# Performance work log

Measured on AMD Instinct MI355X. Metric: run time of the kernel, lower is better.

## Reference

```python
import jax, jax.numpy as jnp
import numpy as np

MODES = 16
WIDTH = 64
SCHMIDT = 8
N_LAYERS = 4


def _spectral_conv(x, wr, wi, modes):
    """Quantum spectral conv: truncated 2D FFT -> complex Schmidt-rank einsum -> inverse FFT.
    x: (B,H,W,C) real. wr, wi: (modes,modes,C,C,S)."""
    b, H, W, C = x.shape
    S = wr.shape[-1]
    # quantum_fourier_modes: keep low (modes x modes) Fourier modes
    x_ft = jnp.fft.fftn(x, axes=(1, 2))[:, :modes, :modes, :]          # (B,m,n,C) complex
    w = wr + 1j * wi                                                     # (m,n,C,C,S)
    # tensor_product_einsum('b...nc,mncos->b...mos')
    out_ft = jnp.einsum('bxnc,mncos->bxmos', x_ft, w)                   # (B,m,m,C,S)
    # recombine Schmidt components (normalized sum over rank)
    out_ft = out_ft.sum(axis=-1) * (1.0 / float(np.sqrt(S)))            # (B,m,m,C)
    full = jnp.zeros((b, H, W, C), dtype=x_ft.dtype).at[:, :modes, :modes, :].set(out_ft)
    # inverse quantum_fourier_modes + .real
    return jnp.fft.ifftn(full, axes=(1, 2)).real


def setup_inputs() -> dict:
    key = jax.random.key(0)
    ks = jax.random.split(key, 12)
    B, H, W, Cin = 16, 128, 128, 3
    sc = 0.02
    inp = {
        'x': jax.random.normal(ks[0], (B, H, W, Cin), jnp.float32),
        'fc_in_w': jax.random.normal(ks[1], (Cin, WIDTH), jnp.float32) * sc,
        'fc_in_b': jnp.zeros((WIDTH,), jnp.float32),
        'wr': jax.random.normal(ks[2], (N_LAYERS, MODES, MODES, WIDTH, WIDTH, SCHMIDT), jnp.float32) * sc,
        'wi': jax.random.normal(ks[3], (N_LAYERS, MODES, MODES, WIDTH, WIDTH, SCHMIDT), jnp.float32) * sc,
        'ww': jax.random.normal(ks[4], (N_LAYERS, WIDTH, WIDTH), jnp.float32) * sc,
        'wb': jnp.zeros((N_LAYERS, WIDTH), jnp.float32),
        'fc1_w': jax.random.normal(ks[5], (WIDTH, 128), jnp.float32) * sc,
        'fc1_b': jnp.zeros((128,), jnp.float32),
        'fc2_w': jax.random.normal(ks[6], (128, 1), jnp.float32) * sc,
        'fc2_b': jnp.zeros((1,), jnp.float32),
    }
    return inp


def reference(x, fc_in_w, fc_in_b, wr, wi, ww, wb, fc1_w, fc1_b, fc2_w, fc2_b) -> jnp.ndarray:
    h = x @ fc_in_w + fc_in_b                                   # (B,H,W,width)
    for i in range(N_LAYERS):
        x1 = _spectral_conv(h, wr[i], wi[i], MODES)             # quantum spectral path
        x2 = h @ ww[i] + wb[i]                                  # pointwise Dense path
        h = jax.nn.gelu(x1 + x2)
    h = jax.nn.gelu(h @ fc1_w + fc1_b)
    return h @ fc2_w + fc2_b                                    # (B,H,W,1)
```

## Files before the change

### kernel.cpp

```cpp
#include <hip/hip_runtime.h>
#include <math.h>


#define TWO_PI_128 0.049087385212340517f

__device__ __forceinline__ float gelu_f(float v) {
  float ex = 1.5957691216057308f * v * fmaf(0.044715f, v * v, 1.0f);
  float e = __expf(fminf(ex, 30.0f));
  float r = __builtin_amdgcn_rcpf(e + 1.0f);
  return fmaf(-v, r, v);
}

__global__ __launch_bounds__(256) void k_fc_in(const float* __restrict__ x,
    const float* __restrict__ w, const float* __restrict__ b,
    float* __restrict__ h) {
  int t = blockIdx.x * 256 + threadIdx.x;
  int pix = t >> 4, c4 = (t & 15) << 2;
  float x0 = x[pix * 3], x1 = x[pix * 3 + 1], x2 = x[pix * 3 + 2];
  float4 acc = *(const float4*)&b[c4];
  float4 w0 = *(const float4*)&w[c4];
  float4 w1 = *(const float4*)&w[64 + c4];
  float4 w2 = *(const float4*)&w[128 + c4];
  acc.x = fmaf(x2, w2.x, fmaf(x1, w1.x, fmaf(x0, w0.x, acc.x)));
  acc.y = fmaf(x2, w2.y, fmaf(x1, w1.y, fmaf(x0, w0.y, acc.y)));
  acc.z = fmaf(x2, w2.z, fmaf(x1, w1.z, fmaf(x0, w0.z, acc.z)));
  acc.w = fmaf(x2, w2.w, fmaf(x1, w1.w, fmaf(x0, w0.w, acc.w)));
  *(float4*)&h[(size_t)pix * 64 + c4] = acc;
}

__global__ __launch_bounds__(256) void k_prep(const float* __restrict__ wr,
    const float* __restrict__ wi, float* __restrict__ Br, float* __restrict__ Bi) {
  int t = blockIdx.x * 256 + threadIdx.x;
  int o = t & 63, c = (t >> 6) & 63, n = (t >> 12) & 15, m = t >> 16;
  const float4* pr = (const float4*)(wr) + (size_t)t * 2;
  float4 a = pr[0], d = pr[1];
  float sr = ((a.x + a.y) + (a.z + a.w)) + ((d.x + d.y) + (d.z + d.w));
  const float4* pi = (const float4*)(wi) + (size_t)t * 2;
  a = pi[0]; d = pi[1];
  float si = ((a.x + a.y) + (a.z + a.w)) + ((d.x + d.y) + (d.z + d.w));
  const float scale = 0.35355339059327373f / 16384.0f;
  int k = n * 64 + c, j = m * 64 + o;
  Br[k * 1024 + j] = sr * scale;
  Bi[k * 1024 + j] = si * scale;
}

__global__ __launch_bounds__(256) void k_dft_y(const float* __restrict__ h,
                                               float2* __restrict__ A1) {
  __shared__ float sh[128 * 64];
  int bx = blockIdx.x;
  const float* src = h + (size_t)bx * 8192;
  for (int i = threadIdx.x; i < 2048; i += 256)
    *(float4*)&sh[i * 4] = *(const float4*)&src[i * 4];
  __syncthreads();
  int c = threadIdx.x & 63, kg = threadIdx.x >> 6;
  float s4r[4][4], s4i[4][4];
  float w4r[4], w4i[4], c4t[4], s4t[4];
  #pragma unroll
  for (int q = 0; q < 4; ++q) {
    int ky = kg + 4 * q;
    __sincosf(-TWO_PI_128 * 4.0f * (float)ky, &s4t[q], &c4t[q]);
    w4r[q] = 1.f; w4i[q] = 0.f;
    #pragma unroll
    for (int p = 0; p < 4; ++p) { s4r[q][p] = 0.f; s4i[q][p] = 0.f; }
  }
  for (int m = 0; m < 32; ++m) {
    float hv[4];
    #pragma unroll
    for (int p = 0; p < 4; ++p) hv[p] = sh[(4 * m + p) * 64 + c];
    #pragma unroll
    for (int q = 0; q < 4; ++q) {
      #pragma unroll
      for (int p = 0; p < 4; ++p) {
        s4r[q][p] = fmaf(hv[p], w4r[q], s4r[q][p]);
        s4i[q][p] = fmaf(hv[p], w4i[q], s4i[q][p]);
      }
      float nw = w4r[q] * c4t[q] - w4i[q] * s4t[q];
      w4i[q] = fmaf(w4i[q], c4t[q], w4r[q] * s4t[q]);
      w4r[q] = nw;
    }
  }
  #pragma unroll
  for (int q = 0; q < 4; ++q) {
    int ky = kg + 4 * q;
    float s1, c1;
    __sincosf(-TWO_PI_128 * (float)ky, &s1, &c1);
    float sr = s4r[q][0], si = s4i[q][0];
    float wr_ = c1, wi_ = s1;
    #pragma unroll
    for (int p = 1; p < 4; ++p) {
      sr = fmaf(s4r[q][p], wr_, sr); sr = fmaf(-s4i[q][p], wi_, sr);
      si = fmaf(s4r[q][p], wi_, si); si = fmaf(s4i[q][p], wr_, si);
      float nw = wr_ * c1 - wi_ * s1;
      wi_ = fmaf(wi_, c1, wr_ * s1);
      wr_ = nw;
    }
    A1[((size_t)bx * 16 + ky) * 64 + c] = make_float2(sr, si);
  }
}

__global__ __launch_bounds__(256) void k_dft_x(const float2* __restrict__ A1,
    float* __restrict__ Ar, float* __restrict__ Ai) {
  __shared__ float2 sh[128 * 32];
  int b = blockIdx.x, ky = blockIdx.y, ch = blockIdx.z;
  int c0 = ch * 32;
  for (int i = threadIdx.x; i < 2048; i += 256) {
    int xx = i >> 4, u = (i & 15) * 2;
    *(float4*)&sh[xx * 32 + u] =
        *(const float4*)&A1[(((size_t)b * 128 + xx) * 16 + ky) * 64 + c0 + u];
  }
  __syncthreads();
  int cl = threadIdx.x & 31, kxg = threadIdx.x >> 5;
  float cs[2], sn[2], wr_[2], wi_[2], sr[2], si[2];
  #pragma unroll
  for (int q = 0; q < 2; ++q) {
    int kx = kxg + 8 * q;
    __sincosf(-TWO_PI_128 * (float)kx, &sn[q], &cs[q]);
    wr_[q] = 1.f; wi_[q] = 0.f; sr[q] = 0.f; si[q] = 0.f;
  }
  for (int xx = 0; xx < 128; ++xx) {
    float2 v = sh[xx * 32 + cl];
    #pragma unroll
    for (int q = 0; q < 2; ++q) {
      sr[q] = fmaf(v.x, wr_[q], sr[q]); sr[q] = fmaf(-v.y, wi_[q], sr[q]);
      si[q] = fmaf(v.x, wi_[q], si[q]); si[q] = fmaf(v.y, wr_[q], si[q]);
      float nw = wr_[q] * cs[q] - wi_[q] * sn[q];
      wi_[q] = fmaf(wi_[q], cs[q], wr_[q] * sn[q]);
      wr_[q] = nw;
    }
  }
  #pragma unroll
  for (int q = 0; q < 2; ++q) {
    int kx = kxg + 8 * q;
    int row = b * 16 + kx, col = ky * 64 + c0 + cl;
    Ar[row * 1024 + col] = sr[q];
    Ai[row * 1024 + col] = si[q];
  }
}

#define CMAC(cr, ci, ax, ay, bx, by)                 \
  cr = fmaf(ax, bx, cr); cr = fmaf(-(ay), by, cr);   \
  ci = fmaf(ax, by, ci); ci = fmaf(ay, bx, ci);

__global__ __launch_bounds__(256) void k_gemm(const float* __restrict__ Ar,
    const float* __restrict__ Ai, const float* __restrict__ Br,
    const float* __restrict__ Bi, float2* __restrict__ Cp) {
  __shared__ float2 As[2][32][34];
  __shared__ float2 Bs[2][32][34];
  int tx = threadIdx.x & 15, ty = threadIdx.x >> 4;
  int row0 = blockIdx.y * 32, col0 = blockIdx.x * 32, kbase = blockIdx.z * 512;
  int ra = threadIdx.x >> 3, k4 = (threadIdx.x & 7) << 2;
  float4 arv, aiv, brv, biv;
  float cr00 = 0, cr01 = 0, cr10 = 0, cr11 = 0;
  float ci00 = 0, ci01 = 0, ci10 = 0, ci11 = 0;
  {
    int gia = (row0 + ra) * 1024 + kbase + k4;
    arv = *(const float4*)&Ar[gia];
    aiv = *(const float4*)&Ai[gia];
    int gib = (kbase + ra) * 1024 + col0 + k4;
    brv = *(const float4*)&Br[gib];
    biv = *(const float4*)&Bi[gib];
    *(float4*)&As[0][ra][k4]     = make_float4(arv.x, aiv.x, arv.y, aiv.y);
    *(float4*)&As[0][ra][k4 + 2] = make_float4(arv.z, aiv.z, arv.w, aiv.w);
    *(float4*)&Bs[0][ra][k4]     = make_float4(brv.x, biv.x, brv.y, biv.y);
    *(float4*)&Bs[0][ra][k4 + 2] = make_float4(brv.z, biv.z, brv.w, biv.w);
  }
  __syncthreads();
  for (int kt = 0; kt < 16; ++kt) {
    if (kt < 15) {
      int k0 = kbase + (kt + 1) * 32;
      int gia = (row0 + ra) * 1024 + k0 + k4;
      arv = *(const float4*)&Ar[gia];
      aiv = *(const float4*)&Ai[gia];
      int gib = (k0 + ra) * 1024 + col0 + k4;
      brv = *(const float4*)&Br[gib];
      biv = *(const float4*)&Bi[gib];
    }
    int cur = kt & 1;
    #pragma unroll 8
    for (int kk2 = 0; kk2 < 16; ++kk2) {
      float4 a0p = *(const float4*)&As[cur][ty * 2][kk2 * 2];
      float4 a1p = *(const float4*)&As[cur][ty * 2 + 1][kk2 * 2];
      float4 b0p = *(const float4*)&Bs[cur][kk2 * 2][tx * 2];
      float4 b1p = *(const float4*)&Bs[cur][kk2 * 2 + 1][tx * 2];
      CMAC(cr00, ci00, a0p.x, a0p.y, b0p.x, b0p.y)
      CMAC(cr01, ci01, a0p.x, a0p.y, b0p.z, b0p.w)
      CMAC(cr10, ci10, a1p.x, a1p.y, b0p.x, b0p.y)
      CMAC(cr11, ci11, a1p.x, a1p.y, b0p.z, b0p.w)
      CMAC(cr00, ci00, a0p.z, a0p.w, b1p.x, b1p.y)
      CMAC(cr01, ci01, a0p.z, a0p.w, b1p.z, b1p.w)
      CMAC(cr10, ci10, a1p.z, a1p.w, b1p.x, b1p.y)
      CMAC(cr11, ci11, a1p.z, a1p.w, b1p.z, b1p.w)
    }
    __syncthreads();
    if (kt < 15) {
      int nxt = cur ^ 1;
      *(float4*)&As[nxt][ra][k4]     = make_float4(arv.x, aiv.x, arv.y, aiv.y);
      *(float4*)&As[nxt][ra][k4 + 2] = make_float4(arv.z, aiv.z, arv.w, aiv.w);
      *(float4*)&Bs[nxt][ra][k4]     = make_float4(brv.x, biv.x, brv.y, biv.y);
      *(float4*)&Bs[nxt][ra][k4 + 2] = make_float4(brv.z, biv.z, brv.w, biv.w);
    }
    __syncthreads();
  }
  int r = row0 + ty * 2, jj = col0 + tx * 2;
  size_t base = ((size_t)blockIdx.z * 256 + r) * 1024 + jj;
  Cp[base]        = make_float2(cr00, ci00);
  Cp[base + 1]    = make_float2(cr01, ci01);
  Cp[base + 1024] = make_float2(cr10, ci10);
  Cp[base + 1025] = make_float2(cr11, ci11);
}

__global__ __launch_bounds__(256) void k_ifft_y(const float2* __restrict__ Cp,
                                                float2* __restrict__ T) {
  __shared__ float2 Cl[1024];
  int b = blockIdx.x >> 4, kx = blockIdx.x & 15;
  int row = b * 16 + kx;
  for (int i = threadIdx.x; i < 512; i += 256) {
    float4 u = *(const float4*)&Cp[(size_t)row * 1024 + i * 2];
    float4 v = *(const float4*)&Cp[(size_t)(256 + row) * 1024 + i * 2];
    *(float4*)&Cl[i * 2] = make_float4(u.x + v.x, u.y + v.y, u.z + v.z, u.w + v.w);
  }
  __syncthreads();
  int c = threadIdx.x & 63, yg = threadIdx.x >> 6;
  for (int y = yg; y < 128; y += 4) {
    float snv, csv;
    __sincosf(TWO_PI_128 * (float)y, &snv, &csv);
    float wr_ = 1.f, wi_ = 0.f, sr = 0.f, si = 0.f;
    #pragma unroll
    for (int ky = 0; ky < 16; ++ky) {
      float2 v = Cl[ky * 64 + c];
      sr = fmaf(v.x, wr_, sr); sr = fmaf(-v.y, wi_, sr);
      si = fmaf(v.x, wi_, si); si = fmaf(v.y, wr_, si);
      float nw = wr_ * csv - wi_ * snv;
      wi_ = fmaf(wi_, csv, wr_ * snv);
      wr_ = nw;
    }
    T[(((size_t)b * 128 + y) * 16 + kx) * 64 + c] = make_float2(sr, si);
  }
}

__global__ __launch_bounds__(256, 4) void k_layer_out(const float* hin,
    const float2* __restrict__ T, const float* __restrict__ ww,
    const float* __restrict__ wb, float* hout) {
  __shared__ alignas(16) float wwT[64 * 68];
  int b = blockIdx.x >> 7, y = blockIdx.x & 127;
  for (int i = threadIdx.x; i < 1024; i += 256) {
    int k = i >> 4, c4 = (i & 15) << 2;
    float4 v = *(const float4*)&ww[k * 64 + c4];
    wwT[(c4 + 0) * 68 + k] = v.x;
    wwT[(c4 + 1) * 68 + k] = v.y;
    wwT[(c4 + 2) * 68 + k] = v.z;
    wwT[(c4 + 3) * 68 + k] = v.w;
  }
  const float2* Tp = T + ((size_t)b * 128 + y) * 1024;
  __syncthreads();
  int ct = threadIdx.x & 7, xg = threadIdx.x >> 3;
  float acc[4][8];
  #pragma unroll
  for (int cc = 0; cc < 8; ++cc) {
    float bv = wb[ct + 8 * cc];
    #pragma unroll
    for (int j = 0; j < 4; ++j) acc[j][cc] = bv;
  }
  #pragma unroll
  for (int kx = 0; kx < 16; ++kx) {
    float tr[8], ti[8];
    #pragma unroll
    for (int cc = 0; cc < 8; ++cc) {
      float2 v = Tp[kx * 64 + ct + 8 * cc];
      tr[cc] = v.x; ti[cc] = v.y;
    }
    float s0v, c0v;
    __sincosf(TWO_PI_128 * (float)(kx * xg), &s0v, &c0v);
    float wr_ = c0v, wi_ = s0v;
    #pragma unroll
    for (int j = 0; j < 4; ++j) {
      #pragma unroll
      for (int cc = 0; cc < 8; ++cc) {
        acc[j][cc] = fmaf(tr[cc], wr_, acc[j][cc]);
        acc[j][cc] = fmaf(-ti[cc], wi_, acc[j][cc]);
      }
      float owr = wr_, owi = wi_;
      if ((kx & 3) == 1)      { wr_ = -owi; wi_ =  owr; }
      else if ((kx & 3) == 2) { wr_ = -owr; wi_ = -owi; }
      else if ((kx & 3) == 3) { wr_ =  owi; wi_ = -owr; }
    }
  }
  const float* hp = hin + (((size_t)b * 128 + xg) * 128 + y) * 64;
  #pragma unroll 1
  for (int kq = 0; kq < 64; kq += 4) {
    float4 wv[8];
    #pragma unroll
    for (int cc = 0; cc < 8; ++cc)
      wv[cc] = *(const float4*)&wwT[(ct + 8 * cc) * 68 + kq];
    #pragma unroll
    for (int j = 0; j < 4; ++j) {
      float4 hv = *(const float4*)&hp[(size_t)j * 262144 + kq];
      #pragma unroll
      for (int cc = 0; cc < 8; ++cc) {
        acc[j][cc] = fmaf(hv.x, wv[cc].x, acc[j][cc]);
        acc[j][cc] = fmaf(hv.y, wv[cc].y, acc[j][cc]);
        acc[j][cc] = fmaf(hv.z, wv[cc].z, acc[j][cc]);
        acc[j][cc] = fmaf(hv.w, wv[cc].w, acc[j][cc]);
      }
    }
  }
  __syncthreads();
  #pragma unroll
  for (int j = 0; j < 4; ++j) {
    int xx = xg + 32 * j;
    size_t base = (((size_t)b * 128 + xx) * 128 + y) * 64 + ct;
    #pragma unroll
    for (int cc = 0; cc < 8; ++cc)
      hout[base + 8 * cc] = gelu_f(acc[j][cc]);
  }
}

__global__ __launch_bounds__(256) void k_final(const float* __restrict__ h,
    const float* __restrict__ w1, const float* __restrict__ b1,
    const float* __restrict__ w2, const float* __restrict__ b2,
    float* __restrict__ out) {
  __shared__ alignas(16) float w1T[128 * 68];
  __shared__ alignas(16) float hl[64 * 68];
  __shared__ float b1s[128];
  __shared__ float w2s[128];
  for (int i = threadIdx.x; i < 8192; i += 256) {
    int k = i >> 7, j = i & 127;
    w1T[j * 68 + k] = w1[i];
  }
  if (threadIdx.x < 128) {
    b1s[threadIdx.x] = b1[threadIdx.x];
    w2s[threadIdx.x] = w2[threadIdx.x];
  }
  int r0 = blockIdx.x * 64;
  for (int i = threadIdx.x; i < 1024; i += 256) {
    int r = i >> 4, kq = (i & 15) * 4;
    float4 v = *(const float4*)&h[(size_t)(r0 + r) * 64 + kq];
    *(float4*)&hl[r * 68 + kq] = v;
  }
  __syncthreads();
  int jt = threadIdx.x & 15, rg = threadIdx.x >> 4;
  float acc[4][8];
  #pragma unroll
  for (int cc = 0; cc < 8; ++cc) {
    float bv = b1s[jt + 16 * cc];
    #pragma unroll
    for (int ii = 0; ii < 4; ++ii) acc[ii][cc] = bv;
  }
  #pragma unroll 1
  for (int kq = 0; kq < 64; kq += 4) {
    float4 hv[4];
    #pragma unroll
    for (int ii = 0; ii < 4; ++ii)
      hv[ii] = *(const float4*)&hl[(rg + 16 * ii) * 68 + kq];
    #pragma unroll
    for (int cc = 0; cc < 8; ++cc) {
      float4 wv = *(const float4*)&w1T[(jt + 16 * cc) * 68 + kq];
      #pragma unroll
      for (int ii = 0; ii < 4; ++ii) {
        acc[ii][cc] = fmaf(hv[ii].x, wv.x, acc[ii][cc]);
        acc[ii][cc] = fmaf(hv[ii].y, wv.y, acc[ii][cc]);
        acc[ii][cc] = fmaf(hv[ii].z, wv.z, acc[ii][cc]);
        acc[ii][cc] = fmaf(hv[ii].w, wv.w, acc[ii][cc]);
      }
    }
  }
  float b2v = b2[0];
  #pragma unroll
  for (int ii = 0; ii < 4; ++ii) {
    float part = 0.f;
    #pragma unroll
    for (int cc = 0; cc < 8; ++cc)
      part = fmaf(gelu_f(acc[ii][cc]), w2s[jt + 16 * cc], part);
    part += __shfl_xor(part, 1, 64);
    part += __shfl_xor(part, 2, 64);
    part += __shfl_xor(part, 4, 64);
    part += __shfl_xor(part, 8, 64);
    if (jt == 0) out[r0 + rg + 16 * ii] = part + b2v;
  }
}

extern "C" void kernel_launch(void* const* d_in, const int* in_sizes, int n_in,
                              void* d_out, int out_size, void* d_ws, size_t ws_size,
                              hipStream_t stream) {
  (void)in_sizes; (void)n_in; (void)out_size; (void)ws_size;
  const float* x      = (const float*)d_in[0];
  const float* fcin_w = (const float*)d_in[1];
  const float* fcin_b = (const float*)d_in[2];
  const float* wr     = (const float*)d_in[3];
  const float* wi     = (const float*)d_in[4];
  const float* ww     = (const float*)d_in[5];
  const float* wb     = (const float*)d_in[6];
  const float* fc1_w  = (const float*)d_in[7];
  const float* fc1_b  = (const float*)d_in[8];
  const float* fc2_w  = (const float*)d_in[9];
  const float* fc2_b  = (const float*)d_in[10];
  float* out = (float*)d_out;

  float*  hA = (float*)d_ws;
  float2* A1 = (float2*)(hA + 16777216);
  float*  Ar = (float*)(A1 + 2097152);
  float*  Ai = Ar + 262144;
  float*  Br = Ai + 262144;
  float*  Bi = Br + 1048576;
  float2* Cp = (float2*)(Bi + 1048576);

  k_fc_in<<<16384, 256, 0, stream>>>(x, fcin_w, fcin_b, hA);
  for (int l = 0; l < 4; ++l) {
    k_prep<<<4096, 256, 0, stream>>>(wr + (size_t)l * 8388608,
                                     wi + (size_t)l * 8388608, Br, Bi);
    k_dft_y<<<2048, 256, 0, stream>>>(hA, A1);
    k_dft_x<<<dim3(16, 16, 2), 256, 0, stream>>>(A1, Ar, Ai);
    k_gemm<<<dim3(32, 8, 2), 256, 0, stream>>>(Ar, Ai, Br, Bi, Cp);
    k_ifft_y<<<256, 256, 0, stream>>>(Cp, A1);
    k_layer_out<<<2048, 256, 0, stream>>>(hA, A1, ww + (size_t)l * 4096,
                                          wb + (size_t)l * 64, hA);
  }
  k_final<<<4096, 256, 0, stream>>>(hA, fc1_w, fc1_b, fc2_w, fc2_b, out);
}
```

Measured before the change: 1.001 ms.

## Enlarge complex GEMM tiles with split-K atomics and widen final MLP block tile

The complex GEMM now uses 64x64 output tiles with a 4x4 per-thread register block and splits K eight ways. Partial sums are accumulated with atomicAdd into a zeroed buffer, which removes the two-slice reduction in k_ifft_y. The final MLP kernel processes 256 rows per block instead of 64, reusing the transposed fc1 weights over more rows. Costs are an extra memset per layer, atomic contention, higher register pressure (launch_bounds 256,1 in k_final), and nondeterministic float summation order.

```diff
diff --git a/kernel.cpp b/kernel.cpp
--- a/kernel.cpp
+++ b/kernel.cpp
@@ -143,70 +143,78 @@
 
 __global__ __launch_bounds__(256) void k_gemm(const float* __restrict__ Ar,
     const float* __restrict__ Ai, const float* __restrict__ Br,
-    const float* __restrict__ Bi, float2* __restrict__ Cp) {
-  __shared__ float2 As[2][32][34];
-  __shared__ float2 Bs[2][32][34];
-  int tx = threadIdx.x & 15, ty = threadIdx.x >> 4;
-  int row0 = blockIdx.y * 32, col0 = blockIdx.x * 32, kbase = blockIdx.z * 512;
-  int ra = threadIdx.x >> 3, k4 = (threadIdx.x & 7) << 2;
-  float4 arv, aiv, brv, biv;
-  float cr00 = 0, cr01 = 0, cr10 = 0, cr11 = 0;
-  float ci00 = 0, ci01 = 0, ci10 = 0, ci11 = 0;
-  {
-    int gia = (row0 + ra) * 1024 + kbase + k4;
-    arv = *(const float4*)&Ar[gia];
-    aiv = *(const float4*)&Ai[gia];
-    int gib = (kbase + ra) * 1024 + col0 + k4;
-    brv = *(const float4*)&Br[gib];
-    biv = *(const float4*)&Bi[gib];
-    *(float4*)&As[0][ra][k4]     = make_float4(arv.x, aiv.x, arv.y, aiv.y);
-    *(float4*)&As[0][ra][k4 + 2] = make_float4(arv.z, aiv.z, arv.w, aiv.w);
-    *(float4*)&Bs[0][ra][k4]     = make_float4(brv.x, biv.x, brv.y, biv.y);
-    *(float4*)&Bs[0][ra][k4 + 2] = make_float4(brv.z, biv.z, brv.w, biv.w);
-  }
-  __syncthreads();
-  for (int kt = 0; kt < 16; ++kt) {
-    if (kt < 15) {
-      int k0 = kbase + (kt + 1) * 32;
-      int gia = (row0 + ra) * 1024 + k0 + k4;
-      arv = *(const float4*)&Ar[gia];
-      aiv = *(const float4*)&Ai[gia];
-      int gib = (k0 + ra) * 1024 + col0 + k4;
-      brv = *(const float4*)&Br[gib];
-      biv = *(const float4*)&Bi[gib];
-    }
+    const float* __restrict__ Bi, float* __restrict__ Cf) {
+  __shared__ float2 As[2][64][34];
+  __shared__ float2 Bs[2][32][66];
+  int t = threadIdx.x;
+  int tx = t & 15, ty = t >> 4;
+  int col0 = blockIdx.x * 64, row0 = blockIdx.y * 64, kb0 = blockIdx.z * 128;
+  int ra = t >> 2, ka8 = (t & 3) * 8;
+  int rb = t >> 3, jb8 = (t & 7) * 8;
+  float4 arv0, arv1, aiv0, aiv1, brv0, brv1, biv0, biv1;
+  float cr[4][4] = {{0,0,0,0},{0,0,0,0},{0,0,0,0},{0,0,0,0}};
+  float ci[4][4] = {{0,0,0,0},{0,0,0,0},{0,0,0,0},{0,0,0,0}};
+
+  auto ldT = [&](int k0) {
+    int g = (row0 + ra) * 1024 + k0 + ka8;
+    arv0 = *(const float4*)&Ar[g]; arv1 = *(const float4*)&Ar[g + 4];
+    aiv0 = *(const float4*)&Ai[g]; aiv1 = *(const float4*)&Ai[g + 4];
+    int gb = (k0 + rb) * 1024 + col0 + jb8;
+    brv0 = *(const float4*)&Br[gb]; brv1 = *(const float4*)&Br[gb + 4];
+    biv0 = *(const float4*)&Bi[gb]; biv1 = *(const float4*)&Bi[gb + 4];
+  };
+  auto stT = [&](int buf) {
+    *(float4*)&As[buf][ra][ka8]     = make_float4(arv0.x, aiv0.x, arv0.y, aiv0.y);
+    *(float4*)&As[buf][ra][ka8 + 2] = make_float4(arv0.z, aiv0.z, arv0.w, aiv0.w);
+    *(float4*)&As[buf][ra][ka8 + 4] = make_float4(arv1.x, aiv1.x, arv1.y, aiv1.y);
+    *(float4*)&As[buf][ra][ka8 + 6] = make_float4(arv1.z, aiv1.z, arv1.w, aiv1.w);
+    *(float4*)&Bs[buf][rb][jb8]     = make_float4(brv0.x, biv0.x, brv0.y, biv0.y);
+    *(float4*)&Bs[buf][rb][jb8 + 2] = make_float4(brv0.z, biv0.z, brv0.w, biv0.w);
+    *(float4*)&Bs[buf][rb][jb8 + 4] = make_float4(brv1.x, biv1.x, brv1.y, biv1.y);
+    *(float4*)&Bs[buf][rb][jb8 + 6] = make_float4(brv1.z, biv1.z, brv1.w, biv1.w);
+  };
+
+  ldT(kb0); stT(0);
+  __syncthreads();
+  for (int kt = 0; kt < 4; ++kt) {
+    if (kt < 3) ldT(kb0 + (kt + 1) * 32);
     int cur = kt & 1;
-    #pragma unroll 8
+    #pragma unroll 4
     for (int kk2 = 0; kk2 < 16; ++kk2) {
-      float4 a0p = *(const float4*)&As[cur][ty * 2][kk2 * 2];
-      float4 a1p = *(const float4*)&As[cur][ty * 2 + 1][kk2 * 2];
-      float4 b0p = *(const float4*)&Bs[cur][kk2 * 2][tx * 2];
-      float4 b1p = *(const float4*)&Bs[cur][kk2 * 2 + 1][tx * 2];
-      CMAC(cr00, ci00, a0p.x, a0p.y, b0p.x, b0p.y)
-      CMAC(cr01, ci01, a0p.x, a0p.y, b0p.z, b0p.w)
-      CMAC(cr10, ci10, a1p.x, a1p.y, b0p.x, b0p.y)
-      CMAC(cr11, ci11, a1p.x, a1p.y, b0p.z, b0p.w)
-      CMAC(cr00, ci00, a0p.z, a0p.w, b1p.x, b1p.y)
-      CMAC(cr01, ci01, a0p.z, a0p.w, b1p.z, b1p.w)
-      CMAC(cr10, ci10, a1p.z, a1p.w, b1p.x, b1p.y)
-      CMAC(cr11, ci11, a1p.z, a1p.w, b1p.z, b1p.w)
+      float4 av[4];
+      #pragma unroll
+      for (int rr = 0; rr < 4; ++rr)
+        av[rr] = *(const float4*)&As[cur][ty * 4 + rr][kk2 * 2];
+      float4 b00 = *(const float4*)&Bs[cur][kk2 * 2][tx * 4];
+      float4 b01 = *(const float4*)&Bs[cur][kk2 * 2][tx * 4 + 2];
+      float4 b10 = *(const float4*)&Bs[cur][kk2 * 2 + 1][tx * 4];
+      float4 b11 = *(const float4*)&Bs[cur][kk2 * 2 + 1][tx * 4 + 2];
+      #pragma unroll
+      for (int rr = 0; rr < 4; ++rr) {
+        CMAC(cr[rr][0], ci[rr][0], av[rr].x, av[rr].y, b00.x, b00.y)
+        CMAC(cr[rr][1], ci[rr][1], av[rr].x, av[rr].y, b00.z, b00.w)
+        CMAC(cr[rr][2], ci[rr][2], av[rr].x, av[rr].y, b01.x, b01.y)
+        CMAC(cr[rr][3], ci[rr][3], av[rr].x, av[rr].y, b01.z, b01.w)
+        CMAC(cr[rr][0], ci[rr][0], av[rr].z, av[rr].w, b10.x, b10.y)
+        CMAC(cr[rr][1], ci[rr][1], av[rr].z, av[rr].w, b10.z, b10.w)
+        CMAC(cr[rr][2], ci[rr][2], av[rr].z, av[rr].w, b11.x, b11.y)
+        CMAC(cr[rr][3], ci[rr][3], av[rr].z, av[rr].w, b11.z, b11.w)
+      }
     }
     __syncthreads();
-    if (kt < 15) {
-      int nxt = cur ^ 1;
-      *(float4*)&As[nxt][ra][k4]     = make_float4(arv.x, aiv.x, arv.y, aiv.y);
-      *(float4*)&As[nxt][ra][k4 + 2] = make_float4(arv.z, aiv.z, arv.w, aiv.w);
-      *(float4*)&Bs[nxt][ra][k4]     = make_float4(brv.x, biv.x, brv.y, biv.y);
-      *(float4*)&Bs[nxt][ra][k4 + 2] = make_float4(brv.z, biv.z, brv.w, biv.w);
-    }
+    if (kt < 3) stT(cur ^ 1);
     __syncthreads();
   }
-  int r = row0 + ty * 2, jj = col0 + tx * 2;
-  size_t base = ((size_t)blockIdx.z * 256 + r) * 1024 + jj;
-  Cp[base]        = make_float2(cr00, ci00);
-  Cp[base + 1]    = make_float2(cr01, ci01);
-  Cp[base + 1024] = make_float2(cr10, ci10);
-  Cp[base + 1025] = make_float2(cr11, ci11);
+  #pragma unroll
+  for (int rr = 0; rr < 4; ++rr) {
+    int r = row0 + ty * 4 + rr;
+    #pragma unroll
+    for (int jj = 0; jj < 4; ++jj) {
+      int j = col0 + tx * 4 + jj;
+      atomicAdd(&Cf[((size_t)r * 1024 + j) * 2],     cr[rr][jj]);
+      atomicAdd(&Cf[((size_t)r * 1024 + j) * 2 + 1], ci[rr][jj]);
+    }
+  }
 }
 
 __global__ __launch_bounds__(256) void k_ifft_y(const float2* __restrict__ Cp,
@@ -214,11 +222,8 @@
   __shared__ float2 Cl[1024];
   int b = blockIdx.x >> 4, kx = blockIdx.x & 15;
   int row = b * 16 + kx;
-  for (int i = threadIdx.x; i < 512; i += 256) {
-    float4 u = *(const float4*)&Cp[(size_t)row * 1024 + i * 2];
-    float4 v = *(const float4*)&Cp[(size_t)(256 + row) * 1024 + i * 2];
-    *(float4*)&Cl[i * 2] = make_float4(u.x + v.x, u.y + v.y, u.z + v.z, u.w + v.w);
-  }
+  for (int i = threadIdx.x; i < 512; i += 256)
+    *(float4*)&Cl[i * 2] = *(const float4*)&Cp[(size_t)row * 1024 + i * 2];
   __syncthreads();
   int c = threadIdx.x & 63, yg = threadIdx.x >> 6;
   for (int y = yg; y < 128; y += 4) {
@@ -315,12 +320,12 @@
   }
 }
 
-__global__ __launch_bounds__(256) void k_final(const float* __restrict__ h,
+__global__ __launch_bounds__(256, 1) void k_final(const float* __restrict__ h,
     const float* __restrict__ w1, const float* __restrict__ b1,
     const float* __restrict__ w2, const float* __restrict__ b2,
     float* __restrict__ out) {
   __shared__ alignas(16) float w1T[128 * 68];
-  __shared__ alignas(16) float hl[64 * 68];
+  __shared__ alignas(16) float hl[256 * 68];
   __shared__ float b1s[128];
   __shared__ float w2s[128];
   for (int i = threadIdx.x; i < 8192; i += 256) {
@@ -331,32 +336,32 @@
     b1s[threadIdx.x] = b1[threadIdx.x];
     w2s[threadIdx.x] = w2[threadIdx.x];
   }
-  int r0 = blockIdx.x * 64;
-  for (int i = threadIdx.x; i < 1024; i += 256) {
+  int r0 = blockIdx.x * 256;
+  for (int i = threadIdx.x; i < 4096; i += 256) {
     int r = i >> 4, kq = (i & 15) * 4;
     float4 v = *(const float4*)&h[(size_t)(r0 + r) * 64 + kq];
     *(float4*)&hl[r * 68 + kq] = v;
   }
   __syncthreads();
   int jt = threadIdx.x & 15, rg = threadIdx.x >> 4;
-  float acc[4][8];
+  float acc[16][8];
   #pragma unroll
   for (int cc = 0; cc < 8; ++cc) {
     float bv = b1s[jt + 16 * cc];
     #pragma unroll
-    for (int ii = 0; ii < 4; ++ii) acc[ii][cc] = bv;
+    for (int ii = 0; ii < 16; ++ii) acc[ii][cc] = bv;
   }
   #pragma unroll 1
   for (int kq = 0; kq < 64; kq += 4) {
-    float4 hv[4];
-    #pragma unroll
-    for (int ii = 0; ii < 4; ++ii)
+    float4 hv[16];
+    #pragma unroll
+    for (int ii = 0; ii < 16; ++ii)
       hv[ii] = *(const float4*)&hl[(rg + 16 * ii) * 68 + kq];
     #pragma unroll
     for (int cc = 0; cc < 8; ++cc) {
       float4 wv = *(const float4*)&w1T[(jt + 16 * cc) * 68 + kq];
       #pragma unroll
-      for (int ii = 0; ii < 4; ++ii) {
+      for (int ii = 0; ii < 16; ++ii) {
         acc[ii][cc] = fmaf(hv[ii].x, wv.x, acc[ii][cc]);
         acc[ii][cc] = fmaf(hv[ii].y, wv.y, acc[ii][cc]);
         acc[ii][cc] = fmaf(hv[ii].z, wv.z, acc[ii][cc]);
@@ -366,7 +371,7 @@
   }
   float b2v = b2[0];
   #pragma unroll
-  for (int ii = 0; ii < 4; ++ii) {
+  for (int ii = 0; ii < 16; ++ii) {
     float part = 0.f;
     #pragma unroll
     for (int cc = 0; cc < 8; ++cc)
@@ -410,10 +415,11 @@
                                      wi + (size_t)l * 8388608, Br, Bi);
     k_dft_y<<<2048, 256, 0, stream>>>(hA, A1);
     k_dft_x<<<dim3(16, 16, 2), 256, 0, stream>>>(A1, Ar, Ai);
-    k_gemm<<<dim3(32, 8, 2), 256, 0, stream>>>(Ar, Ai, Br, Bi, Cp);
+    hipMemsetAsync(Cp, 0, 262144 * sizeof(float2), stream);
+    k_gemm<<<dim3(16, 4, 8), 256, 0, stream>>>(Ar, Ai, Br, Bi, (float*)Cp);
     k_ifft_y<<<256, 256, 0, stream>>>(Cp, A1);
     k_layer_out<<<2048, 256, 0, stream>>>(hA, A1, ww + (size_t)l * 4096,
                                           wb + (size_t)l * 64, hA);
   }
-  k_final<<<4096, 256, 0, stream>>>(hA, fc1_w, fc1_b, fc2_w, fc2_b, out);
-}
+  k_final<<<1024, 256, 0, stream>>>(hA, fc1_w, fc1_b, fc2_w, fc2_b, out);
+}
```

Measured after the change: 1.465 ms. 46.3% more time.
